# Performance work log

Measured on AMD Instinct MI355X. Metric: run time of the kernel, lower is better.

The kernel has to match this reference:

```python
import jax, jax.numpy as jnp
import numpy as np
from jax import lax

FACTOR = 2
FIR = (1.0, 3.0, 3.0, 1.0)


def _fir_kernel():
    k1 = jnp.array(FIR, dtype=jnp.float32)
    k = jnp.outer(k1, k1)
    k = k / jnp.sum(k)
    return k * (FACTOR ** 2)  # gain=1, factor=2 -> x4


def _upfirdn2d(x, kernel, up, down, pad):
    # x: [N, C, H, W]; kernel: [kh, kw]; faithful to upfirdn2d_native:
    # upsample by zero-insertion (lhs_dilation), pad, convolve with flipped
    # kernel (F.conv2d is correlation of flipped kernel == true convolution),
    # then downsample by striding. lax.conv_general_dilated is correlation,
    # so pass the flipped kernel.
    C = x.shape[1]
    kflip = kernel[::-1, ::-1]
    w = jnp.tile(kflip[None, None], (C, 1, 1, 1))  # depthwise [C,1,kh,kw]
    return lax.conv_general_dilated(
        x, w,
        window_strides=(down, down),
        padding=[(pad[0], pad[1]), (pad[0], pad[1])],
        lhs_dilation=(up, up),
        feature_group_count=C,
        dimension_numbers=("NCHW", "OIHW", "NCHW"),
    )


def setup_inputs() -> dict:
    key = jax.random.key(0)
    k1, k2, k3 = jax.random.split(key, 3)
    N, C, H, W = 8, 256, 64, 64
    outC = 256
    hidden_states = jax.random.normal(k1, (N, C, H, W), dtype=jnp.float32)
    weight = jax.random.normal(k2, (outC, C, 3, 3), dtype=jnp.float32) * 0.05
    bias = jax.random.normal(k3, (outC,), dtype=jnp.float32)
    return {"hidden_states": hidden_states, "weight": weight, "bias": bias}


def reference(hidden_states, weight, bias):
    # FirUpsample2D.forward with use_conv=True, fir_kernel=(1,3,3,1), factor=2.
    k = _fir_kernel()  # [4, 4]
    convH, convW = weight.shape[2], weight.shape[3]
    pad_value = k.shape[0] - FACTOR - (convW - 1)  # = 0 here

    # The torch code flips+channel-swaps the weight then calls conv_transpose2d
    # (which itself flips and channel-swaps); the two cancel, so the net op is
    # plain cross-correlation of the ORIGINAL weight over the factor-dilated
    # input with (kH-1) padding on each side (output_padding == 0).
    x = lax.conv_general_dilated(
        hidden_states, weight,
        window_strides=(1, 1),
        padding=[(convH - 1, convH - 1), (convW - 1, convW - 1)],
        lhs_dilation=(FACTOR, FACTOR),
        dimension_numbers=("NCHW", "OIHW", "NCHW"),
    )  # [N, outC, (H-1)*2+3, (W-1)*2+3]

    out = _upfirdn2d(
        x, k, up=1, down=1,
        pad=((pad_value + 1) // 2 + FACTOR - 1, pad_value // 2 + 1),
    )  # [N, outC, 2H, 2W]

    return out + bias[None, :, None, None]
```

## Files before the change

kernel.cpp:

```cpp
#include <hip/hip_runtime.h>
#include <cstdint>
#include <cstddef>

typedef _Float16 f16;
typedef _Float16 f16x8 __attribute__((ext_vector_type(8)));
typedef float f32x4 __attribute__((ext_vector_type(4)));

#define AS1 __attribute__((address_space(1)))
#define AS3 __attribute__((address_space(3)))

__device__ __forceinline__ void gl_lds16(const void* g, void* l) {
  __builtin_amdgcn_global_load_lds((AS1 void*)g, (AS3 void*)l, 16u, 0, 0u);
}

__constant__ float c_tab[2][3][3] = {
  {{0.75f, 0.25f, 0.00f}, {0.25f, 0.75f, 0.75f}, {0.00f, 0.00f, 0.25f}},
  {{0.25f, 0.00f, 0.00f}, {0.75f, 0.75f, 0.25f}, {0.00f, 0.25f, 0.75f}}
};

__global__ __launch_bounds__(256) void build_E_k(const float* __restrict__ W,
                                                 f16* __restrict__ Et) {
  const int oc = blockIdx.x;
  const int ic = threadIdx.x;
  float w[9];
  const float* wp = W + ((size_t)oc * 256 + ic) * 9;
#pragma unroll
  for (int t = 0; t < 9; ++t) w[t] = wp[t];
#pragma unroll
  for (int py = 0; py < 2; ++py)
#pragma unroll
    for (int px = 0; px < 2; ++px) {
      const int p = py * 2 + px;
#pragma unroll
      for (int ay = 0; ay < 3; ++ay)
#pragma unroll
        for (int ax = 0; ax < 3; ++ax) {
          float s = 0.f;
#pragma unroll
          for (int iy = 0; iy < 3; ++iy)
#pragma unroll
            for (int ix = 0; ix < 3; ++ix)
              s += w[iy * 3 + ix] * c_tab[py][ay][iy] * c_tab[px][ax][ix];
          Et[(size_t)(oc * 4 + p) * 2304 + (ay * 3 + ax) * 256 + ic] = (f16)s;
        }
    }
}

__global__ __launch_bounds__(256) void zero_A_k(uint4* __restrict__ p) {
  p[(size_t)blockIdx.x * 256 + threadIdx.x] = make_uint4(0u, 0u, 0u, 0u);
}

__global__ __launch_bounds__(256) void fill_A_k(const float* __restrict__ In,
                                                f16* __restrict__ Ah) {
  const int bid = blockIdx.x;
  const int icc = bid & 7;
  const int y = (bid >> 3) & 63;
  const int n = bid >> 9;
  const int ic0 = icc * 32;
  __shared__ float tile[32][65];
  const int tid = threadIdx.x;
  const int xl = tid & 63, icl4 = tid >> 6;
  const float* src = In + (((size_t)(n * 256 + ic0)) * 64 + y) * 64;
#pragma unroll
  for (int i = 0; i < 8; ++i) {
    const int icl = i * 4 + icl4;
    tile[icl][xl] = src[(size_t)icl * 4096 + xl];
  }
  __syncthreads();
  const int icl = tid & 31, x8 = tid >> 5;
  f16* dst = Ah + ((size_t)(n * 66 + y + 1) * 66 + 1) * 256 + ic0;
#pragma unroll
  for (int i = 0; i < 8; ++i) {
    const int x = i * 8 + x8;
    dst[(size_t)x * 256 + icl] = (f16)tile[icl][x];
  }
}

#define BM 128
#define BN 128
#define BK 32
#define KSTEPS 72

__global__ __launch_bounds__(256) void gemm_k(const f16* __restrict__ Ah,
                                              const f16* __restrict__ Et,
                                              const float* __restrict__ bias,
                                              float* __restrict__ out) {
  __shared__ __align__(16) f16 lA[BM * BK];
  __shared__ __align__(16) f16 lB[BN * BK];
  const int tid = threadIdx.x;
  const int wave = tid >> 6;
  const int lane = tid & 63;
  const int bid = blockIdx.x;
  const int nt = bid & 7;
  const int mt = bid >> 3;
  const int m0 = mt * BM;
  const int jj0 = nt * BN;
  const int n = m0 >> 12;
  const int y0 = (m0 >> 6) & 63;

  const int arow = wave * 32 + (lane >> 2);
  const int y_r = y0 + (arow >> 6);
  const int x_r = arow & 63;
  const f16* pA = Ah + ((size_t)(n * 66 + y_r + 1) * 66 + (x_r + 1)) * 256 + (lane & 3) * 8;
  const f16* pB = Et + (size_t)(jj0 + wave * 32 + (lane >> 2)) * 2304 + (lane & 3) * 8;
  f16* dA0 = lA + (wave * 32) * BK;
  f16* dA1 = lA + (wave * 32 + 16) * BK;
  f16* dB0 = lB + (wave * 32) * BK;
  f16* dB1 = lB + (wave * 32 + 16) * BK;

  const int wm = wave >> 1, wn = wave & 1;
  const int lr = lane & 15;
  const int lk = (lane >> 4) * 8;
  int aoff[4], boff[4];
#pragma unroll
  for (int i = 0; i < 4; ++i) {
    aoff[i] = (wm * 64 + i * 16 + lr) * BK + lk;
    boff[i] = (wn * 64 + i * 16 + lr) * BK + lk;
  }

  const f32x4 vzero = {0.f, 0.f, 0.f, 0.f};
  f32x4 acc[4][4];
#pragma unroll
  for (int i = 0; i < 4; ++i)
#pragma unroll
    for (int j = 0; j < 4; ++j) acc[i][j] = vzero;

  for (int ks = 0; ks < KSTEPS; ++ks) {
    const int k0 = ks * BK;
    const int r = k0 >> 8;
    const int ic0 = k0 & 255;
    const int ayt = r / 3, axt = r - ayt * 3;
    const int delta = ((ayt - 1) * 66 + (axt - 1)) * 256 + ic0;

    __syncthreads();
    gl_lds16(pA + delta, dA0);
    gl_lds16(pA + delta + 16 * 256, dA1);
    gl_lds16(pB + k0, dB0);
    gl_lds16(pB + k0 + 16 * 2304, dB1);
    __syncthreads();

    f16x8 af[4], bf[4];
#pragma unroll
    for (int mi = 0; mi < 4; ++mi) af[mi] = *(const f16x8*)(lA + aoff[mi]);
#pragma unroll
    for (int ni = 0; ni < 4; ++ni) bf[ni] = *(const f16x8*)(lB + boff[ni]);
#pragma unroll
    for (int mi = 0; mi < 4; ++mi)
#pragma unroll
      for (int ni = 0; ni < 4; ++ni)
        acc[mi][ni] = __builtin_amdgcn_mfma_f32_16x16x32_f16(af[mi], bf[ni], acc[mi][ni], 0, 0, 0);
  }

  const int yw = y0 + wm;
#pragma unroll
  for (int ni = 0; ni < 4; ++ni) {
    const int jj = jj0 + wn * 64 + ni * 16 + lr;
    const int oc = jj >> 2;
    const int py = (jj >> 1) & 1, px = jj & 1;
    const float bv = bias[oc];
    const int oy = 2 * yw + py;
    float* orow = out + ((size_t)(n * 256 + oc) * 128 + oy) * 128;
#pragma unroll
    for (int mi = 0; mi < 4; ++mi) {
      const int xb = mi * 16 + ((lane >> 4) << 2);
#pragma unroll
      for (int v = 0; v < 4; ++v) {
        orow[2 * (xb + v) + px] = acc[mi][ni][v] + bv;
      }
    }
  }
}

__global__ __launch_bounds__(256) void fallback_k(const float* __restrict__ In,
                                                  const float* __restrict__ W,
                                                  const float* __restrict__ bias,
                                                  float* __restrict__ out) {
  const size_t idx = (size_t)blockIdx.x * 256 + threadIdx.x;
  const int ox = (int)(idx & 127), oy = (int)((idx >> 7) & 127);
  const int oc = (int)((idx >> 14) & 255);
  const int n = (int)(idx >> 22);
  const int px = ox & 1, py = oy & 1;
  const int x = ox >> 1, y = oy >> 1;
  float cy[3][3], cx[3][3];
#pragma unroll
  for (int a = 0; a < 3; ++a)
#pragma unroll
    for (int i = 0; i < 3; ++i) {
      cy[a][i] = c_tab[py][a][i];
      cx[a][i] = c_tab[px][a][i];
    }
  float acc = 0.f;
  const float* wbase = W + (size_t)oc * 2304;
  for (int ic = 0; ic < 256; ++ic) {
    const float* ib = In + (((size_t)(n * 256 + ic)) * 64 + y) * 64 + x;
    float pin[3][3];
#pragma unroll
    for (int ay = 0; ay < 3; ++ay) {
      const int yy = y + ay - 1;
#pragma unroll
      for (int ax = 0; ax < 3; ++ax) {
        const int xx = x + ax - 1;
        pin[ay][ax] = (yy >= 0 && yy < 64 && xx >= 0 && xx < 64)
                          ? ib[(ay - 1) * 64 + (ax - 1)] : 0.f;
      }
    }
    const float* w = wbase + ic * 9;
    float U[3][3];
#pragma unroll
    for (int ay = 0; ay < 3; ++ay)
#pragma unroll
      for (int ix = 0; ix < 3; ++ix)
        U[ay][ix] = cx[0][ix] * pin[ay][0] + cx[1][ix] * pin[ay][1] + cx[2][ix] * pin[ay][2];
#pragma unroll
    for (int iy = 0; iy < 3; ++iy)
#pragma unroll
      for (int ix = 0; ix < 3; ++ix) {
        const float V = cy[0][iy] * U[0][ix] + cy[1][iy] * U[1][ix] + cy[2][iy] * U[2][ix];
        acc += w[iy * 3 + ix] * V;
      }
  }
  out[idx] = acc + bias[oc];
}

extern "C" void kernel_launch(void* const* d_in, const int* in_sizes, int n_in,
                              void* d_out, int out_size, void* d_ws, size_t ws_size,
                              hipStream_t stream) {
  const float* In = (const float*)d_in[0];
  const float* W = (const float*)d_in[1];
  const float* bias = (const float*)d_in[2];
  float* out = (float*)d_out;

  const size_t E_BYTES = (size_t)1024 * 2304 * 2;
  const size_t A_BYTES = (size_t)8 * 66 * 66 * 256 * 2;

  if (ws_size >= E_BYTES + A_BYTES) {
    f16* Et = (f16*)d_ws;
    f16* Ah = (f16*)((char*)d_ws + E_BYTES);
    build_E_k<<<256, 256, 0, stream>>>(W, Et);
    zero_A_k<<<4356, 256, 0, stream>>>((uint4*)Ah);
    fill_A_k<<<4096, 256, 0, stream>>>(In, Ah);
    gemm_k<<<2048, 256, 0, stream>>>(Ah, Et, bias, out);
  } else {
    fallback_k<<<131072, 256, 0, stream>>>(In, W, bias, out);
  }
}
```

Measured before the change: 390.2 us.

## Fuse prep kernels and reuse halo A tile across horizontal taps in GEMM

Merges weight-expansion, padding-zeroing and input transpose into one prep kernel that writes only the halo zeros instead of clearing the whole buffer. The GEMM now loads a 2-row by 66-column A strip per (channel chunk, ay) once and reuses it for all three ax taps, while the E matrix is relaid out as [c][ay][ax][jj][32] so B for the three taps loads in one staged step. This cuts global-to-LDS traffic for A and the number of barriers per K step. In exchange it uses more LDS per block and relies on tricky index math for the halo tile.

```diff
diff --git a/kernel.cpp b/kernel.cpp
--- a/kernel.cpp
+++ b/kernel.cpp
@@ -18,105 +18,125 @@
   {{0.25f, 0.00f, 0.00f}, {0.75f, 0.75f, 0.25f}, {0.00f, 0.25f, 0.75f}}
 };
 
-__global__ __launch_bounds__(256) void build_E_k(const float* __restrict__ W,
-                                                 f16* __restrict__ Et) {
-  const int oc = blockIdx.x;
-  const int ic = threadIdx.x;
-  float w[9];
-  const float* wp = W + ((size_t)oc * 256 + ic) * 9;
-#pragma unroll
-  for (int t = 0; t < 9; ++t) w[t] = wp[t];
-#pragma unroll
-  for (int py = 0; py < 2; ++py)
-#pragma unroll
-    for (int px = 0; px < 2; ++px) {
-      const int p = py * 2 + px;
-#pragma unroll
-      for (int ay = 0; ay < 3; ++ay)
-#pragma unroll
-        for (int ax = 0; ax < 3; ++ax) {
-          float s = 0.f;
-#pragma unroll
-          for (int iy = 0; iy < 3; ++iy)
-#pragma unroll
-            for (int ix = 0; ix < 3; ++ix)
-              s += w[iy * 3 + ix] * c_tab[py][ay][iy] * c_tab[px][ax][ix];
-          Et[(size_t)(oc * 4 + p) * 2304 + (ay * 3 + ax) * 256 + ic] = (f16)s;
-        }
-    }
-}
-
-__global__ __launch_bounds__(256) void zero_A_k(uint4* __restrict__ p) {
-  p[(size_t)blockIdx.x * 256 + threadIdx.x] = make_uint4(0u, 0u, 0u, 0u);
-}
-
-__global__ __launch_bounds__(256) void fill_A_k(const float* __restrict__ In,
-                                                f16* __restrict__ Ah) {
-  const int bid = blockIdx.x;
-  const int icc = bid & 7;
-  const int y = (bid >> 3) & 63;
-  const int n = bid >> 9;
-  const int ic0 = icc * 32;
-  __shared__ float tile[32][65];
+__global__ __launch_bounds__(256) void prep_k(const float* __restrict__ W,
+                                              const float* __restrict__ In,
+                                              f16* __restrict__ Et,
+                                              f16* __restrict__ Ah) {
+  const int b = blockIdx.x;
   const int tid = threadIdx.x;
-  const int xl = tid & 63, icl4 = tid >> 6;
-  const float* src = In + (((size_t)(n * 256 + ic0)) * 64 + y) * 64;
-#pragma unroll
-  for (int i = 0; i < 8; ++i) {
-    const int icl = i * 4 + icl4;
-    tile[icl][xl] = src[(size_t)icl * 4096 + xl];
-  }
-  __syncthreads();
-  const int icl = tid & 31, x8 = tid >> 5;
-  f16* dst = Ah + ((size_t)(n * 66 + y + 1) * 66 + 1) * 256 + ic0;
-#pragma unroll
-  for (int i = 0; i < 8; ++i) {
-    const int x = i * 8 + x8;
-    dst[(size_t)x * 256 + icl] = (f16)tile[icl][x];
-  }
-}
-
-#define BM 128
-#define BN 128
-#define BK 32
-#define KSTEPS 72
+  if (b < 256) {
+    const int oc = b;
+    const int ic = tid;
+    const int c = ic >> 5, icl = ic & 31;
+    float w[9];
+    const float* wp = W + ((size_t)oc * 256 + ic) * 9;
+#pragma unroll
+    for (int t = 0; t < 9; ++t) w[t] = wp[t];
+#pragma unroll
+    for (int py = 0; py < 2; ++py)
+#pragma unroll
+      for (int px = 0; px < 2; ++px) {
+        const int jj = oc * 4 + py * 2 + px;
+#pragma unroll
+        for (int ay = 0; ay < 3; ++ay)
+#pragma unroll
+          for (int ax = 0; ax < 3; ++ax) {
+            float s = 0.f;
+#pragma unroll
+            for (int iy = 0; iy < 3; ++iy)
+#pragma unroll
+              for (int ix = 0; ix < 3; ++ix)
+                s += w[iy * 3 + ix] * c_tab[py][ay][iy] * c_tab[px][ax][ix];
+            Et[((size_t)(((c * 3 + ay) * 3 + ax) * 1024 + jj)) * 32 + icl] = (f16)s;
+          }
+      }
+  } else {
+    const int bid2 = b - 256;
+    const int icc = bid2 & 7;
+    const int v = bid2 >> 3;
+    const int n = v / 66;
+    const int yp = v - n * 66;
+    const int ic0 = icc * 32;
+    const int icl = tid & 31, x8 = tid >> 5;
+    f16* rowbase = Ah + ((size_t)(n * 66 + yp) * 66) * 256 + ic0;
+    if (yp == 0 || yp == 65) {
+#pragma unroll
+      for (int i = 0; i < 9; ++i) {
+        const int xp = i * 8 + x8;
+        if (xp < 66) rowbase[(size_t)xp * 256 + icl] = (f16)0.f;
+      }
+    } else {
+      const int y = yp - 1;
+      __shared__ float tile[32][65];
+      const int xl = tid & 63, icl4 = tid >> 6;
+      const float* src = In + (((size_t)(n * 256 + ic0)) * 64 + y) * 64;
+#pragma unroll
+      for (int i = 0; i < 8; ++i) {
+        const int icl_ = i * 4 + icl4;
+        tile[icl_][xl] = src[(size_t)icl_ * 4096 + xl];
+      }
+      __syncthreads();
+      f16* dst = rowbase + 256;
+#pragma unroll
+      for (int i = 0; i < 8; ++i) {
+        const int x = i * 8 + x8;
+        dst[(size_t)x * 256 + icl] = (f16)tile[icl][x];
+      }
+      if (x8 == 0) {
+        rowbase[icl] = (f16)0.f;
+        rowbase[(size_t)65 * 256 + icl] = (f16)0.f;
+      }
+    }
+  }
+}
 
 __global__ __launch_bounds__(256) void gemm_k(const f16* __restrict__ Ah,
                                               const f16* __restrict__ Et,
                                               const float* __restrict__ bias,
                                               float* __restrict__ out) {
-  __shared__ __align__(16) f16 lA[BM * BK];
-  __shared__ __align__(16) f16 lB[BN * BK];
+  __shared__ __align__(16) f16 lA[4224];
+  __shared__ __align__(16) f16 lB[12288];
   const int tid = threadIdx.x;
   const int wave = tid >> 6;
   const int lane = tid & 63;
   const int bid = blockIdx.x;
   const int nt = bid & 7;
   const int mt = bid >> 3;
-  const int m0 = mt * BM;
-  const int jj0 = nt * BN;
+  const int m0 = mt * 128;
+  const int jj0 = nt * 128;
   const int n = m0 >> 12;
   const int y0 = (m0 >> 6) & 63;
 
-  const int arow = wave * 32 + (lane >> 2);
-  const int y_r = y0 + (arow >> 6);
-  const int x_r = arow & 63;
-  const f16* pA = Ah + ((size_t)(n * 66 + y_r + 1) * 66 + (x_r + 1)) * 256 + (lane & 3) * 8;
-  const f16* pB = Et + (size_t)(jj0 + wave * 32 + (lane >> 2)) * 2304 + (lane & 3) * 8;
-  f16* dA0 = lA + (wave * 32) * BK;
-  f16* dA1 = lA + (wave * 32 + 16) * BK;
-  f16* dB0 = lB + (wave * 32) * BK;
-  f16* dB1 = lB + (wave * 32 + 16) * BK;
+  int goA[2];
+#pragma unroll
+  for (int i = 0; i < 2; ++i) {
+    const int s = wave * 2 + i;
+    const int u = s * 16 + (lane >> 2);
+    const int row = (u >= 66) ? 1 : 0;
+    const int x = u - 66 * row;
+    goA[i] = ((row * 66 + x) * 256 + (lane & 3) * 8) * 2;
+  }
+  const int goAt = ((66 + 62 + (lane >> 2)) * 256 + (lane & 3) * 8) * 2;
+  int goB[6];
+#pragma unroll
+  for (int j = 0; j < 6; ++j) {
+    const int t = wave + 4 * j;
+    const int ax = t >> 3, sub = t & 7;
+    goB[j] = (ax * 32768 + (sub * 16 + (lane >> 2)) * 32 + (lane & 3) * 8) * 2;
+  }
+  char* const lAb = (char*)lA;
+  char* const lBb = (char*)lB;
+  char* const dA0 = lAb + (wave * 2 + 0) * 1024;
+  char* const dA1 = lAb + (wave * 2 + 1) * 1024;
+  char* const dAt = lAb + 8192;
 
   const int wm = wave >> 1, wn = wave & 1;
   const int lr = lane & 15;
-  const int lk = (lane >> 4) * 8;
-  int aoff[4], boff[4];
-#pragma unroll
-  for (int i = 0; i < 4; ++i) {
-    aoff[i] = (wm * 64 + i * 16 + lr) * BK + lk;
-    boff[i] = (wn * 64 + i * 16 + lr) * BK + lk;
-  }
+  const int base_a = wm * 4224 + lr * 64 + (lane >> 4) * 16;
+  const int base_b = (wn * 64 + lr) * 64 + (lane >> 4) * 16;
+
+  const char* const aN = (const char*)Ah + (size_t)(n * 66 + y0) * 33792;
+  const char* const bE = (const char*)Et + (size_t)jj0 * 64;
 
   const f32x4 vzero = {0.f, 0.f, 0.f, 0.f};
   f32x4 acc[4][4];
@@ -125,30 +145,38 @@
 #pragma unroll
     for (int j = 0; j < 4; ++j) acc[i][j] = vzero;
 
-  for (int ks = 0; ks < KSTEPS; ++ks) {
-    const int k0 = ks * BK;
-    const int r = k0 >> 8;
-    const int ic0 = k0 & 255;
-    const int ayt = r / 3, axt = r - ayt * 3;
-    const int delta = ((ayt - 1) * 66 + (axt - 1)) * 256 + ic0;
-
-    __syncthreads();
-    gl_lds16(pA + delta, dA0);
-    gl_lds16(pA + delta + 16 * 256, dA1);
-    gl_lds16(pB + k0, dB0);
-    gl_lds16(pB + k0 + 16 * 2304, dB1);
-    __syncthreads();
-
-    f16x8 af[4], bf[4];
-#pragma unroll
-    for (int mi = 0; mi < 4; ++mi) af[mi] = *(const f16x8*)(lA + aoff[mi]);
-#pragma unroll
-    for (int ni = 0; ni < 4; ++ni) bf[ni] = *(const f16x8*)(lB + boff[ni]);
-#pragma unroll
-    for (int mi = 0; mi < 4; ++mi)
-#pragma unroll
-      for (int ni = 0; ni < 4; ++ni)
-        acc[mi][ni] = __builtin_amdgcn_mfma_f32_16x16x32_f16(af[mi], bf[ni], acc[mi][ni], 0, 0, 0);
+#pragma unroll 1
+  for (int c = 0; c < 8; ++c) {
+#pragma unroll 1
+    for (int ay = 0; ay < 3; ++ay) {
+      const char* aP = aN + ay * 33792 + c * 64;
+      const char* bP = bE + (size_t)(c * 3 + ay) * 196608;
+
+      __syncthreads();
+      gl_lds16(aP + goA[0], dA0);
+      gl_lds16(aP + goA[1], dA1);
+      if (wave == 3 && lane < 16) gl_lds16(aP + goAt, dAt);
+#pragma unroll
+      for (int j = 0; j < 6; ++j) gl_lds16(bP + goB[j], lBb + (wave + 4 * j) * 1024);
+      __syncthreads();
+
+#pragma unroll
+      for (int ax = 0; ax < 3; ++ax) {
+        f16x8 af[4], bf[4];
+#pragma unroll
+        for (int mi = 0; mi < 4; ++mi)
+          af[mi] = *(const f16x8*)(lAb + base_a + (mi * 16 + ax) * 64);
+#pragma unroll
+        for (int ni = 0; ni < 4; ++ni)
+          bf[ni] = *(const f16x8*)(lBb + base_b + ax * 8192 + ni * 1024);
+#pragma unroll
+        for (int mi = 0; mi < 4; ++mi)
+#pragma unroll
+          for (int ni = 0; ni < 4; ++ni)
+            acc[mi][ni] =
+                __builtin_amdgcn_mfma_f32_16x16x32_f16(af[mi], bf[ni], acc[mi][ni], 0, 0, 0);
+      }
+    }
   }
 
   const int yw = y0 + wm;
@@ -236,9 +264,7 @@
   if (ws_size >= E_BYTES + A_BYTES) {
     f16* Et = (f16*)d_ws;
     f16* Ah = (f16*)((char*)d_ws + E_BYTES);
-    build_E_k<<<256, 256, 0, stream>>>(W, Et);
-    zero_A_k<<<4356, 256, 0, stream>>>((uint4*)Ah);
-    fill_A_k<<<4096, 256, 0, stream>>>(In, Ah);
+    prep_k<<<256 + 4224, 256, 0, stream>>>(W, In, Et, Ah);
     gemm_k<<<2048, 256, 0, stream>>>(Ah, Et, bias, out);
   } else {
     fallback_k<<<131072, 256, 0, stream>>>(In, W, bias, out);
```

Result: faster. 336.3 us (-13.8%).
